# Kernel optimization log

Measured on AMD Instinct MI355X. Metric: run time of the kernel, lower is better.

Reference implementation:

```python
import jax, jax.numpy as jnp
import numpy as np

N, H, W, KB, CTRL, MEM, L, NMOD = 256, 14, 14, 512, 512, 512, 8, 9
TEMP = 1.0
EPS = 1e-12


def _l2norm(x):
    # torch F.normalize(p=2, dim=-1, eps=1e-12)
    return x / jnp.maximum(jnp.linalg.norm(x, axis=-1, keepdims=True), EPS)


def _spatial_softmax(att):  # [N,H,W,1]
    n = att.shape[0]
    return jax.nn.softmax(att.reshape(n, -1), axis=1).reshape(att.shape)


def _extract_softmax_avg(kb, att_raw):  # -> [N,KB]
    return (kb * _spatial_softmax(att_raw)).sum((1, 2))


def _move_bw(ptr):
    # conv1d with kernel [0,0,1], pad 1 => shift left (pop); guard keeps mass at slot 0
    new = jnp.pad(ptr[:, 1:], ((0, 0), (0, 1)))
    return new.at[:, 0].add(ptr[:, 0])


def _move_fw(ptr):
    # conv1d with kernel [1,0,0], pad 1 => shift right (push); guard keeps mass at slot L-1
    new = jnp.pad(ptr[:, :-1], ((0, 0), (1, 0)))
    return new.at[:, -1].add(ptr[:, -1])


def _read(stk, ptr):  # [N,H,W,L],[N,L] -> [N,H,W,1]
    return (stk * ptr[:, None, None, :]).sum(-1, keepdims=True)


def _write(stk, ptr, att):
    p = ptr[:, None, None, :]
    return att * p + stk * (1.0 - p)


def _sharpen(ptr):
    return jax.nn.softmax(ptr / TEMP, axis=1)


def setup_inputs() -> dict:
    key = jax.random.key(0)
    ks = jax.random.split(key, 16)

    def lin(k, fan_in, shape):
        return (jax.random.normal(k, shape, jnp.float32) / np.sqrt(fan_in)).astype(jnp.float32)

    u_ptr = jax.random.uniform(ks[0], (N, L), jnp.float32)
    u_mod = jax.random.uniform(ks[1], (N, NMOD), jnp.float32)
    C2 = 2 * KB + CTRL
    return {
        "control_state": jax.random.normal(ks[2], (N, CTRL), jnp.float32),
        "kb_batch": jax.random.normal(ks[3], (N, H, W, KB), jnp.float32),
        "module_prob": u_mod / u_mod.sum(1, keepdims=True),
        "mem_prev": jax.random.normal(ks[4], (N, MEM), jnp.float32),
        "att_stack_prev": jax.random.uniform(ks[5], (N, H, W, L), jnp.float32),
        "stack_ptr_prev": u_ptr / u_ptr.sum(1, keepdims=True),
        "find_ci_w": lin(ks[6], CTRL, (CTRL, KB)), "find_ci_b": jnp.zeros((KB,), jnp.float32),
        "find_conv_w": lin(ks[7], KB, (KB, 1)), "find_conv_b": jnp.zeros((1,), jnp.float32),
        "transform_ci_w": lin(ks[8], CTRL, (CTRL, KB)), "transform_ci_b": jnp.zeros((KB,), jnp.float32),
        "transform_conv_w": lin(ks[9], KB, (KB, 1)), "transform_conv_b": jnp.zeros((1,), jnp.float32),
        "scene_conv_w": lin(ks[10], KB, (KB, 1)), "scene_conv_b": jnp.zeros((1,), jnp.float32),
        "describeone_ci_w": lin(ks[11], CTRL, (CTRL, KB)), "describeone_ci_b": jnp.zeros((KB,), jnp.float32),
        "describeone_mem_w": lin(ks[12], C2, (C2, MEM)), "describeone_mem_b": jnp.zeros((MEM,), jnp.float32),
        "describetwo_ci_w": lin(ks[13], CTRL, (CTRL, KB)), "describetwo_ci_b": jnp.zeros((KB,), jnp.float32),
        "describetwo_mem_w": lin(ks[14], C2, (C2, MEM)), "describetwo_mem_b": jnp.zeros((MEM,), jnp.float32),
    }


def reference(control_state, kb_batch, module_prob, mem_prev, att_stack_prev, stack_ptr_prev,
              find_ci_w, find_ci_b, find_conv_w, find_conv_b,
              transform_ci_w, transform_ci_b, transform_conv_w, transform_conv_b,
              scene_conv_w, scene_conv_b,
              describeone_ci_w, describeone_ci_b, describeone_mem_w, describeone_mem_b,
              describetwo_ci_w, describetwo_ci_b, describetwo_mem_w, describetwo_mem_b):
    mem_zero = jnp.zeros_like(mem_prev)

    def NoOp(stk, ptr):
        return stk, ptr, mem_prev

    def Find(stk, ptr):
        c = control_state @ find_ci_w + find_ci_b  # [N,KB]
        elt = _l2norm(kb_batch * c[:, None, None, :])
        att = elt @ find_conv_w + find_conv_b  # 1x1 conv on channels-last -> [N,H,W,1]
        ptr = _move_fw(ptr)
        return _write(stk, ptr, att), ptr, mem_zero

    def Transform(stk, ptr):
        att_in = _read(stk, ptr)
        c = control_state @ transform_ci_w + transform_ci_b
        kb_att = _extract_softmax_avg(kb_batch, att_in)
        elt = _l2norm(kb_batch * c[:, None, None, :] * kb_att[:, None, None, :])
        att = elt @ transform_conv_w + transform_conv_b
        return _write(stk, ptr, att), ptr, mem_zero

    def And(stk, ptr):
        att2 = _read(stk, ptr)
        ptr = _move_bw(ptr)
        att1 = _read(stk, ptr)
        return _write(stk, ptr, jnp.minimum(att1, att2)), ptr, mem_zero

    def Or(stk, ptr):
        att2 = _read(stk, ptr)
        ptr = _move_bw(ptr)
        att1 = _read(stk, ptr)
        return _write(stk, ptr, jnp.maximum(att1, att2)), ptr, mem_zero

    def Filter(stk, ptr):
        stk, ptr, _ = Find(stk, ptr)
        stk, ptr, _ = And(stk, ptr)
        return stk, ptr, mem_zero

    def Scene(stk, ptr):
        att = _l2norm(kb_batch) @ scene_conv_w + scene_conv_b
        ptr = _move_fw(ptr)
        return _write(stk, ptr, att), ptr, mem_zero

    def DescribeOne(stk, ptr):
        att_in = _read(stk, ptr)
        c = control_state @ describeone_ci_w + describeone_ci_b
        kb_att = _extract_softmax_avg(kb_batch, att_in)
        elt = _l2norm(c * kb_att)
        mem = jnp.concatenate([control_state, elt, kb_att], axis=1) @ describeone_mem_w + describeone_mem_b
        return stk, ptr, mem

    def DescribeTwo(stk, ptr):
        att2 = _read(stk, ptr)
        ptr = _move_bw(ptr)
        att1 = _read(stk, ptr)
        c = control_state @ describetwo_ci_w + describetwo_ci_b
        kb_att1 = _extract_softmax_avg(kb_batch, att1)
        kb_att2 = _extract_softmax_avg(kb_batch, att2)
        elt = _l2norm(c * kb_att1 * kb_att2)
        mem = jnp.concatenate([control_state, elt, kb_att1], axis=1) @ describetwo_mem_w + describetwo_mem_b
        stk = _write(stk, ptr, jnp.minimum(att1, att2))
        return stk, ptr, mem

    funcs = [NoOp, Find, Transform, Filter, And, Or, Scene, DescribeOne, DescribeTwo]
    res = [f(att_stack_prev, stack_ptr_prev) for f in funcs]  # fixed small set of modules
    stks = jnp.stack([r[0] for r in res], axis=-1)  # [N,H,W,L,M]
    ptrs = jnp.stack([r[1] for r in res], axis=-1)  # [N,L,M]
    mems = jnp.stack([r[2] for r in res], axis=-1)  # [N,MEM,M]
    att_stack_avg = (module_prob[:, None, None, None, :] * stks).sum(-1)
    stack_ptr_avg = _sharpen((module_prob[:, None, :] * ptrs).sum(-1))
    mem_avg = (module_prob[:, None, :] * mems).sum(-1)
    return att_stack_avg, stack_ptr_avg, mem_avg
```

## Files before the change

kernel.cpp:

```cpp
#include <hip/hip_runtime.h>
#include <math.h>

constexpr int   NB   = 256;
constexpr int   HW   = 196;
constexpr int   KBC  = 512;
constexpr int   LSZ  = 8;
constexpr float EPSF = 1e-12f;

constexpr size_t S_ATT    = (size_t)NB * HW;
constexpr size_t OFF_ATT1 = 0;
constexpr size_t OFF_ATT2 = OFF_ATT1 + S_ATT;
constexpr size_t OFF_W1   = OFF_ATT2 + S_ATT;
constexpr size_t OFF_W2   = OFF_W1   + S_ATT;
constexpr size_t OFF_AF   = OFF_W2   + S_ATT;
constexpr size_t OFF_AT   = OFF_AF   + S_ATT;
constexpr size_t OFF_AS   = OFF_AT   + S_ATT;
constexpr size_t OFF_GP1  = OFF_AS   + S_ATT;
constexpr size_t OFF_KP   = OFF_GP1  + (size_t)4*NB*2048;
constexpr size_t OFF_A1   = OFF_KP   + (size_t)4*NB*1024;
constexpr size_t OFF_A2   = OFF_A1   + (size_t)NB*1536;
constexpr size_t OFF_G    = OFF_A2   + (size_t)NB*1536;
constexpr size_t OFF_P2   = OFF_G    + (size_t)NB*512;
constexpr size_t OFF_PF   = OFF_P2   + (size_t)16*NB*512;
constexpr size_t OFF_PB   = OFF_PF   + (size_t)NB*LSZ;
constexpr size_t OFF_PFB  = OFF_PB   + (size_t)NB*LSZ;
constexpr size_t OFF_SF2  = OFF_PFB  + (size_t)NB*LSZ;
constexpr size_t OFF_SFFB = OFF_SF2  + NB;
constexpr size_t WS_FLOATS= OFF_SFFB + NB;

static __device__ __forceinline__ float4 ld4(const float* p) {
    return *reinterpret_cast<const float4*>(p);
}

__global__ __launch_bounds__(256) void k_front(
    const float* __restrict__ stk, const float* __restrict__ ptrp,
    float* __restrict__ att1g, float* __restrict__ att2g,
    float* __restrict__ w1g, float* __restrict__ w2g,
    float* __restrict__ fws, float* __restrict__ bws, float* __restrict__ fbws,
    float* __restrict__ sf2ws, float* __restrict__ sffbws,
    const float* __restrict__ control,
    const float* __restrict__ B0, const float* __restrict__ B1,
    const float* __restrict__ B2, const float* __restrict__ B3,
    float* __restrict__ GP1)
{
    __shared__ float red[256];
    __shared__ float As[16][68];
    __shared__ float Bs[16][68];
    const int t = threadIdx.x;

    if (blockIdx.x < 256) {
        const int n = blockIdx.x;
        float pp[8], f[8], b[8], fb[8];
#pragma unroll
        for (int l = 0; l < 8; ++l) pp[l] = ptrp[n*8 + l];
        f[0] = 0.f;
#pragma unroll
        for (int l = 1; l < 8; ++l) f[l] = pp[l-1];
        f[7] += pp[7];
#pragma unroll
        for (int l = 0; l < 7; ++l) b[l] = pp[l+1];
        b[7] = 0.f;
        b[0] += pp[0];
#pragma unroll
        for (int l = 0; l < 7; ++l) fb[l] = f[l+1];
        fb[7] = 0.f;
        fb[0] += f[0];

        if (t == 0) {
            float sf2 = 0.f, sffb = 0.f;
#pragma unroll
            for (int l = 0; l < 8; ++l) {
                fws[n*8+l] = f[l]; bws[n*8+l] = b[l]; fbws[n*8+l] = fb[l];
                sf2  += f[l]*f[l];
                sffb += f[l]*fb[l];
            }
            sf2ws[n] = sf2; sffbws[n] = sffb;
        }

        float a1 = 0.f, a2 = 0.f;
        if (t < HW) {
            const float* sp = stk + ((size_t)n*HW + t) * 8;
            float4 v0 = ld4(sp), v1 = ld4(sp + 4);
            float s[8] = {v0.x, v0.y, v0.z, v0.w, v1.x, v1.y, v1.z, v1.w};
#pragma unroll
            for (int l = 0; l < 8; ++l) {
                a2 = fmaf(s[l], pp[l], a2);
                a1 = fmaf(s[l],  b[l], a1);
            }
            att1g[n*HW + t] = a1;
            att2g[n*HW + t] = a2;
        }

        red[t] = (t < HW) ? a1 : -3.0e38f;
        __syncthreads();
        for (int off = 128; off > 0; off >>= 1) { if (t < off) red[t] = fmaxf(red[t], red[t+off]); __syncthreads(); }
        const float m1 = red[0];
        __syncthreads();
        float e1 = (t < HW) ? __expf(a1 - m1) : 0.f;
        red[t] = e1;
        __syncthreads();
        for (int off = 128; off > 0; off >>= 1) { if (t < off) red[t] += red[t+off]; __syncthreads(); }
        const float s1 = red[0];
        __syncthreads();
        if (t < HW) w1g[n*HW + t] = e1 / s1;

        red[t] = (t < HW) ? a2 : -3.0e38f;
        __syncthreads();
        for (int off = 128; off > 0; off >>= 1) { if (t < off) red[t] = fmaxf(red[t], red[t+off]); __syncthreads(); }
        const float m2 = red[0];
        __syncthreads();
        float e2 = (t < HW) ? __expf(a2 - m2) : 0.f;
        red[t] = e2;
        __syncthreads();
        for (int off = 128; off > 0; off >>= 1) { if (t < off) red[t] += red[t+off]; __syncthreads(); }
        const float s2 = red[0];
        __syncthreads();
        if (t < HW) w2g[n*HW + t] = e2 / s2;
        return;
    }

    const int idx = blockIdx.x - 256;
    const int bn = (idx & 31) * 64;
    const int bm = ((idx >> 5) & 3) * 64;
    const int ks = idx >> 7;
    const int mat = bn >> 9;
    const float* B = (mat == 0) ? B0 : (mat == 1) ? B1 : (mat == 2) ? B2 : B3;
    const int kbase = ks * 128;
    const int bcol = bn & 511;

    const int tx = t & 15, ty = t >> 4;
    float acc[4][4] = {};
    const int ar = t >> 2, ac4 = (t & 3) * 4;
    const int br = t >> 4, bc4 = (t & 15) * 4;
    const float* Aptr = control + (size_t)(bm + ar) * 512 + kbase + ac4;
    const float* Bptr = B + (size_t)(kbase + br) * 512 + bcol + bc4;

    float4 aR = ld4(Aptr), bR = ld4(Bptr);
    for (int tile = 0; tile < 8; ++tile) {
        As[ac4+0][ar] = aR.x; As[ac4+1][ar] = aR.y; As[ac4+2][ar] = aR.z; As[ac4+3][ar] = aR.w;
        *reinterpret_cast<float4*>(&Bs[br][bc4]) = bR;
        __syncthreads();
        if (tile + 1 < 8) {
            aR = ld4(Aptr + (tile+1)*16);
            bR = ld4(Bptr + (size_t)(tile+1)*16*512);
        }
#pragma unroll
        for (int k = 0; k < 16; ++k) {
            float4 ra = *reinterpret_cast<const float4*>(&As[k][ty*4]);
            float4 rb = *reinterpret_cast<const float4*>(&Bs[k][tx*4]);
            const float av[4] = {ra.x, ra.y, ra.z, ra.w};
            const float bv[4] = {rb.x, rb.y, rb.z, rb.w};
#pragma unroll
            for (int i = 0; i < 4; ++i)
#pragma unroll
                for (int j = 0; j < 4; ++j)
                    acc[i][j] = fmaf(av[i], bv[j], acc[i][j]);
        }
        __syncthreads();
    }
#pragma unroll
    for (int i = 0; i < 4; ++i) {
        float4 v = make_float4(acc[i][0], acc[i][1], acc[i][2], acc[i][3]);
        *reinterpret_cast<float4*>(&GP1[((size_t)ks*NB + bm + ty*4 + i) * 2048 + bn + tx*4]) = v;
    }
}

__global__ __launch_bounds__(256) void k_kbA(
    const float* __restrict__ kb, const float* __restrict__ GP1,
    const float* __restrict__ find_ci_b,
    const float* __restrict__ w_find, const float* __restrict__ b_find,
    const float* __restrict__ w_scene, const float* __restrict__ b_scene,
    const float* __restrict__ w1g, const float* __restrict__ w2g,
    float* __restrict__ aF, float* __restrict__ aS, float* __restrict__ kpart)
{
    const int blk = blockIdx.x;
    const int n = blk >> 2, sp = blk & 3;
    const int t = threadIdx.x, wv = t >> 6, lane = t & 63;
    const int k0 = lane * 8;
    const int p0 = sp * 49;

    __shared__ float w1s[49], w2s[49];
    __shared__ float kred[4][1024];
    if (t < 49) { w1s[t] = w1g[n*HW + p0 + t]; w2s[t] = w2g[n*HW + p0 + t]; }
    __syncthreads();

    float cf[8], wf[8], wsc[8];
    {
        const float* gp = GP1 + (size_t)n*2048 + k0;
        float4 a0 = ld4(gp),            a1 = ld4(gp + 4);
        float4 b0 = ld4(gp + 524288),   b1 = ld4(gp + 524288 + 4);
        float4 c0 = ld4(gp + 1048576),  c1 = ld4(gp + 1048576 + 4);
        float4 d0 = ld4(gp + 1572864),  d1 = ld4(gp + 1572864 + 4);
        float4 e0 = ld4(find_ci_b + k0), e1 = ld4(find_ci_b + k0 + 4);
        cf[0]=a0.x+b0.x+c0.x+d0.x+e0.x; cf[1]=a0.y+b0.y+c0.y+d0.y+e0.y;
        cf[2]=a0.z+b0.z+c0.z+d0.z+e0.z; cf[3]=a0.w+b0.w+c0.w+d0.w+e0.w;
        cf[4]=a1.x+b1.x+c1.x+d1.x+e1.x; cf[5]=a1.y+b1.y+c1.y+d1.y+e1.y;
        cf[6]=a1.z+b1.z+c1.z+d1.z+e1.z; cf[7]=a1.w+b1.w+c1.w+d1.w+e1.w;
        float4 f0 = ld4(w_find + k0), f1 = ld4(w_find + k0 + 4);
        wf[0]=f0.x; wf[1]=f0.y; wf[2]=f0.z; wf[3]=f0.w; wf[4]=f1.x; wf[5]=f1.y; wf[6]=f1.z; wf[7]=f1.w;
        float4 g0 = ld4(w_scene + k0), g1 = ld4(w_scene + k0 + 4);
        wsc[0]=g0.x; wsc[1]=g0.y; wsc[2]=g0.z; wsc[3]=g0.w; wsc[4]=g1.x; wsc[5]=g1.y; wsc[6]=g1.z; wsc[7]=g1.w;
    }
    const float bf = b_find[0], bs = b_scene[0];

    float k1a[8] = {0,0,0,0,0,0,0,0};
    float k2a[8] = {0,0,0,0,0,0,0,0};

    const float* src0 = kb + (((size_t)n*HW + p0 + wv) * KBC + k0);
    float4 v0 = ld4(src0), v1 = ld4(src0 + 4);
    for (int pl = wv; pl < 49; pl += 4) {
        float4 n0, n1;
        if (pl + 4 < 49) {
            const float* ns = kb + (((size_t)n*HW + p0 + pl + 4) * KBC + k0);
            n0 = ld4(ns); n1 = ld4(ns + 4);
        }
        float kv[8] = {v0.x, v0.y, v0.z, v0.w, v1.x, v1.y, v1.z, v1.w};
        float sA = 0.f, sB = 0.f, sE = 0.f, sF = 0.f;
#pragma unroll
        for (int j = 0; j < 8; ++j) {
            const float t1 = kv[j] * cf[j];
            sA = fmaf(t1, t1, sA);
            sB = fmaf(t1, wf[j], sB);
            sE = fmaf(kv[j], kv[j], sE);
            sF = fmaf(kv[j], wsc[j], sF);
        }
        const float w1p = w1s[pl], w2p = w2s[pl];
#pragma unroll
        for (int j = 0; j < 8; ++j) {
            k1a[j] = fmaf(w1p, kv[j], k1a[j]);
            k2a[j] = fmaf(w2p, kv[j], k2a[j]);
        }
#pragma unroll
        for (int m = 1; m < 64; m <<= 1) {
            sA += __shfl_xor(sA, m);
            sB += __shfl_xor(sB, m);
            sE += __shfl_xor(sE, m);
            sF += __shfl_xor(sF, m);
        }
        if (lane == 0) {
            const size_t p = (size_t)n*HW + p0 + pl;
            aF[p] = sB / fmaxf(sqrtf(sA), EPSF) + bf;
            aS[p] = sF / fmaxf(sqrtf(sE), EPSF) + bs;
        }
        v0 = n0; v1 = n1;
    }
#pragma unroll
    for (int j = 0; j < 8; ++j) { kred[wv][k0 + j] = k1a[j]; kred[wv][512 + k0 + j] = k2a[j]; }
    __syncthreads();
    for (int idx = t; idx < 1024; idx += 256) {
        const float s = kred[0][idx] + kred[1][idx] + kred[2][idx] + kred[3][idx];
        kpart[((size_t)sp*NB + n) * 1024 + idx] = s;
    }
}

__global__ __launch_bounds__(256) void k_elt(
    const float* __restrict__ kpart, const float* __restrict__ GP1,
    const float* __restrict__ tr_ci_b, const float* __restrict__ d1_ci_b,
    const float* __restrict__ d2_ci_b,
    const float* __restrict__ control, const float* __restrict__ prob,
    float* __restrict__ g, float* __restrict__ A1, float* __restrict__ A2)
{
    const int n = blockIdx.x;
    const int t = threadIdx.x;
    __shared__ float k1s[512], k2s[512];
    for (int idx = t; idx < 512; idx += 256) {
        float s1 = 0.f, s2 = 0.f;
#pragma unroll
        for (int sp = 0; sp < 4; ++sp) {
            const float* base = kpart + ((size_t)sp*NB + n) * 1024;
            s1 += base[idx];
            s2 += base[512 + idx];
        }
        k1s[idx] = s1; k2s[idx] = s2;
    }
    __syncthreads();

    float v1[2], v2[2];
    float sum1 = 0.f, sum2 = 0.f;
#pragma unroll
    for (int i = 0; i < 2; ++i) {
        const int k = t + i*256;
        const float* gp = GP1 + (size_t)n*2048 + k;
        const float ct  = gp[512]  + gp[524288+512]  + gp[1048576+512]  + gp[1572864+512]  + tr_ci_b[k];
        const float cd1 = gp[1024] + gp[524288+1024] + gp[1048576+1024] + gp[1572864+1024] + d1_ci_b[k];
        const float cd2 = gp[1536] + gp[524288+1536] + gp[1048576+1536] + gp[1572864+1536] + d2_ci_b[k];
        g[(size_t)n*512 + k] = ct * k2s[k];
        v1[i] = cd1 * k2s[k];
        v2[i] = cd2 * k1s[k] * k2s[k];
        sum1 = fmaf(v1[i], v1[i], sum1);
        sum2 = fmaf(v2[i], v2[i], sum2);
    }
    __shared__ float r1[256], r2[256];
    r1[t] = sum1; r2[t] = sum2;
    __syncthreads();
    for (int off = 128; off > 0; off >>= 1) {
        if (t < off) { r1[t] += r1[t+off]; r2[t] += r2[t+off]; }
        __syncthreads();
    }
    const float n1 = fmaxf(sqrtf(r1[0]), EPSF);
    const float n2 = fmaxf(sqrtf(r2[0]), EPSF);
    const float p7 = prob[n*9 + 7], p8 = prob[n*9 + 8];
#pragma unroll
    for (int i = 0; i < 2; ++i) {
        const int k = t + i*256;
        const float c = control[(size_t)n*512 + k];
        A1[(size_t)n*1536 + k]        = p7 * c;
        A1[(size_t)n*1536 + 512 + k]  = p7 * v1[i] / n1;
        A1[(size_t)n*1536 + 1024 + k] = p7 * k2s[k];
        A2[(size_t)n*1536 + k]        = p8 * c;
        A2[(size_t)n*1536 + 512 + k]  = p8 * v2[i] / n2;
        A2[(size_t)n*1536 + 1024 + k] = p8 * k1s[k];
    }
}

__global__ __launch_bounds__(256) void k_mid(
    const float* __restrict__ kb, const float* __restrict__ g,
    const float* __restrict__ w_tr, const float* __restrict__ b_tr,
    float* __restrict__ aT,
    const float* __restrict__ A1, const float* __restrict__ A2,
    const float* __restrict__ W1, const float* __restrict__ W2,
    float* __restrict__ P2)
{
    __shared__ float As[16][68];
    __shared__ float Bs[16][68];
    const int t = threadIdx.x;
    const int g3 = blockIdx.x / 3, r3 = blockIdx.x % 3;

    if (r3 != 0) {
        const int kidx = g3 * 2 + (r3 - 1);
        const int n = kidx >> 2, sp = kidx & 3;
        const int wv = t >> 6, lane = t & 63;
        const int k0 = lane * 8;
        const int p0 = sp * 49;
        float gv[8], wt[8];
        {
            float4 a0 = ld4(g + (size_t)n*512 + k0), a1 = ld4(g + (size_t)n*512 + k0 + 4);
            gv[0]=a0.x; gv[1]=a0.y; gv[2]=a0.z; gv[3]=a0.w; gv[4]=a1.x; gv[5]=a1.y; gv[6]=a1.z; gv[7]=a1.w;
            float4 b0 = ld4(w_tr + k0), b1 = ld4(w_tr + k0 + 4);
            wt[0]=b0.x; wt[1]=b0.y; wt[2]=b0.z; wt[3]=b0.w; wt[4]=b1.x; wt[5]=b1.y; wt[6]=b1.z; wt[7]=b1.w;
        }
        const float bt = b_tr[0];
        const float* src0 = kb + (((size_t)n*HW + p0 + wv) * KBC + k0);
        float4 v0 = ld4(src0), v1 = ld4(src0 + 4);
        for (int pl = wv; pl < 49; pl += 4) {
            float4 n0, n1;
            if (pl + 4 < 49) {
                const float* ns = kb + (((size_t)n*HW + p0 + pl + 4) * KBC + k0);
                n0 = ld4(ns); n1 = ld4(ns + 4);
            }
            float kv[8] = {v0.x, v0.y, v0.z, v0.w, v1.x, v1.y, v1.z, v1.w};
            float sC = 0.f, sD = 0.f;
#pragma unroll
            for (int j = 0; j < 8; ++j) {
                const float u = kv[j] * gv[j];
                sC = fmaf(u, u, sC);
                sD = fmaf(u, wt[j], sD);
            }
#pragma unroll
            for (int m = 1; m < 64; m <<= 1) { sC += __shfl_xor(sC, m); sD += __shfl_xor(sD, m); }
            if (lane == 0) aT[(size_t)n*HW + p0 + pl] = sD / fmaxf(sqrtf(sC), EPSF) + bt;
            v0 = n0; v1 = n1;
        }
        return;
    }

    const int idx = g3;
    const int bn = (idx & 7) * 64;
    const int bm = ((idx >> 3) & 3) * 64;
    const int ks = idx >> 5;
    const int mat = ks >> 3;
    const float* A = mat ? A2 : A1;
    const float* B = mat ? W2 : W1;
    const int kbase = ks * 192 - mat * 1536;

    const int tx = t & 15, ty = t >> 4;
    float acc[4][4] = {};
    const int ar = t >> 2, ac4 = (t & 3) * 4;
    const int br = t >> 4, bc4 = (t & 15) * 4;
    const float* Aptr = A + (size_t)(bm + ar) * 1536 + kbase + ac4;
    const float* Bptr = B + (size_t)(kbase + br) * 512 + bn + bc4;

    float4 aR = ld4(Aptr), bR = ld4(Bptr);
    for (int tile = 0; tile < 12; ++tile) {
        As[ac4+0][ar] = aR.x; As[ac4+1][ar] = aR.y; As[ac4+2][ar] = aR.z; As[ac4+3][ar] = aR.w;
        *reinterpret_cast<float4*>(&Bs[br][bc4]) = bR;
        __syncthreads();
        if (tile + 1 < 12) {
            aR = ld4(Aptr + (tile+1)*16);
            bR = ld4(Bptr + (size_t)(tile+1)*16*512);
        }
#pragma unroll
        for (int k = 0; k < 16; ++k) {
            float4 ra = *reinterpret_cast<const float4*>(&As[k][ty*4]);
            float4 rb = *reinterpret_cast<const float4*>(&Bs[k][tx*4]);
            const float av[4] = {ra.x, ra.y, ra.z, ra.w};
            const float bv[4] = {rb.x, rb.y, rb.z, rb.w};
#pragma unroll
            for (int i = 0; i < 4; ++i)
#pragma unroll
                for (int j = 0; j < 4; ++j)
                    acc[i][j] = fmaf(av[i], bv[j], acc[i][j]);
        }
        __syncthreads();
    }
#pragma unroll
    for (int i = 0; i < 4; ++i) {
        float4 v = make_float4(acc[i][0], acc[i][1], acc[i][2], acc[i][3]);
        *reinterpret_cast<float4*>(&P2[((size_t)ks*NB + bm + ty*4 + i) * 512 + bn + tx*4]) = v;
    }
}

__global__ __launch_bounds__(256) void k_back(
    const float* __restrict__ P2, const float* __restrict__ memprev,
    const float* __restrict__ prob,
    const float* __restrict__ mb1, const float* __restrict__ mb2,
    float* __restrict__ out_mem,
    const float* __restrict__ stk, const float* __restrict__ ptrp,
    const float* __restrict__ att1g, const float* __restrict__ att2g,
    const float* __restrict__ aFg, const float* __restrict__ aTg, const float* __restrict__ aSg,
    const float* __restrict__ fws, const float* __restrict__ bws, const float* __restrict__ fbws,
    const float* __restrict__ sf2ws, const float* __restrict__ sffbws,
    float* __restrict__ out_att, float* __restrict__ out_ptr)
{
    const int t = threadIdx.x;
    if (blockIdx.x < 128) {
        const size_t q = ((size_t)blockIdx.x * 256 + t) * 4;
        const int n = (int)(q >> 9), j = (int)(q & 511);
        const float p0 = prob[n*9 + 0], p7 = prob[n*9 + 7], p8 = prob[n*9 + 8];
        float4 s = ld4(P2 + q);
#pragma unroll
        for (int sp = 1; sp < 16; ++sp) {
            float4 v = ld4(P2 + (size_t)sp*131072 + q);
            s.x += v.x; s.y += v.y; s.z += v.z; s.w += v.w;
        }
        float4 mp = ld4(memprev + q);
        float4 w1 = ld4(mb1 + j), w2 = ld4(mb2 + j);
        float4 o;
        o.x = p0*mp.x + s.x + p7*w1.x + p8*w2.x;
        o.y = p0*mp.y + s.y + p7*w1.y + p8*w2.y;
        o.z = p0*mp.z + s.z + p7*w1.z + p8*w2.z;
        o.w = p0*mp.w + s.w + p7*w1.w + p8*w2.w;
        *reinterpret_cast<float4*>(&out_mem[q]) = o;
        return;
    }

    const int n = blockIdx.x - 128;
    __shared__ float pp[8], f[8], b[8], fb[8], pr[9], sc2[2];
    if (t < 8) { pp[t] = ptrp[n*8+t]; f[t] = fws[n*8+t]; b[t] = bws[n*8+t]; fb[t] = fbws[n*8+t]; }
    if (t < 9) pr[t] = prob[n*9+t];
    if (t == 0) { sc2[0] = sf2ws[n]; sc2[1] = sffbws[n]; }
    __syncthreads();

    if (t < HW) {
        const size_t p = (size_t)n*HW + t;
        const float* spt = stk + p*8;
        float4 v0 = ld4(spt), v1 = ld4(spt+4);
        float s[8] = {v0.x, v0.y, v0.z, v0.w, v1.x, v1.y, v1.z, v1.w};
        const float a1 = att1g[p], a2 = att2g[p];
        const float vaF = aFg[p], vaT = aTg[p], vaS = aSg[p];
        const float mn = fminf(a1, a2), mx = fmaxf(a1, a2);
        float rf = 0.f, rf2 = 0.f, rfb = 0.f, rffb = 0.f;
#pragma unroll
        for (int l = 0; l < 8; ++l) {
            rf   = fmaf(s[l], f[l],        rf);
            rf2  = fmaf(s[l], f[l]*f[l],   rf2);
            rfb  = fmaf(s[l], fb[l],       rfb);
            rffb = fmaf(s[l], f[l]*fb[l],  rffb);
        }
        const float att2p = vaF*sc2[0] + rf  - rf2;
        const float att1p = vaF*sc2[1] + rfb - rffb;
        const float mnF = fminf(att1p, att2p);
        const float c48 = pr[4] + pr[8];
        float o[8];
#pragma unroll
        for (int l = 0; l < 8; ++l) {
            const float sl = s[l];
            const float stkF = vaF*f[l] + sl*(1.f - f[l]);
            float r = (pr[0] + pr[7]) * sl;
            r = fmaf(pr[1], stkF, r);
            r = fmaf(pr[2], vaT*pp[l] + sl*(1.f - pp[l]), r);
            r = fmaf(pr[3], mnF*fb[l] + stkF*(1.f - fb[l]), r);
            r = fmaf(c48,   mn*b[l] + sl*(1.f - b[l]), r);
            r = fmaf(pr[5], mx*b[l] + sl*(1.f - b[l]), r);
            r = fmaf(pr[6], vaS*f[l] + sl*(1.f - f[l]), r);
            o[l] = r;
        }
        *reinterpret_cast<float4*>(out_att + p*8)     = make_float4(o[0], o[1], o[2], o[3]);
        *reinterpret_cast<float4*>(out_att + p*8 + 4) = make_float4(o[4], o[5], o[6], o[7]);
    }

    if (t == 0) {
        const float cpp = pr[0] + pr[2] + pr[7];
        const float cf  = pr[1] + pr[6];
        const float cb  = pr[4] + pr[5] + pr[8];
        float pa[8];
        float m = -3.0e38f;
#pragma unroll
        for (int l = 0; l < 8; ++l) {
            pa[l] = cpp*pp[l] + cf*f[l] + cb*b[l] + pr[3]*fb[l];
            m = fmaxf(m, pa[l]);
        }
        float ssum = 0.f;
#pragma unroll
        for (int l = 0; l < 8; ++l) { pa[l] = __expf(pa[l] - m); ssum += pa[l]; }
#pragma unroll
        for (int l = 0; l < 8; ++l) out_ptr[n*8 + l] = pa[l] / ssum;
    }
}

extern "C" void kernel_launch(void* const* d_in, const int* in_sizes, int n_in,
                              void* d_out, int out_size, void* d_ws, size_t ws_size,
                              hipStream_t stream)
{
    (void)in_sizes; (void)n_in; (void)out_size;
    const float* control = (const float*)d_in[0];
    const float* kb      = (const float*)d_in[1];
    const float* prob    = (const float*)d_in[2];
    const float* memprev = (const float*)d_in[3];
    const float* stk     = (const float*)d_in[4];
    const float* ptrp    = (const float*)d_in[5];
    const float* find_w  = (const float*)d_in[6];
    const float* find_b  = (const float*)d_in[7];
    const float* findc_w = (const float*)d_in[8];
    const float* findc_b = (const float*)d_in[9];
    const float* tr_w    = (const float*)d_in[10];
    const float* tr_b    = (const float*)d_in[11];
    const float* trc_w   = (const float*)d_in[12];
    const float* trc_b   = (const float*)d_in[13];
    const float* sc_w    = (const float*)d_in[14];
    const float* sc_b    = (const float*)d_in[15];
    const float* d1_w    = (const float*)d_in[16];
    const float* d1_b    = (const float*)d_in[17];
    const float* d1m_w   = (const float*)d_in[18];
    const float* d1m_b   = (const float*)d_in[19];
    const float* d2_w    = (const float*)d_in[20];
    const float* d2_b    = (const float*)d_in[21];
    const float* d2m_w   = (const float*)d_in[22];
    const float* d2m_b   = (const float*)d_in[23];

    if (ws_size < WS_FLOATS * sizeof(float)) return;

    float* ws    = (float*)d_ws;
    float* att1g = ws + OFF_ATT1;
    float* att2g = ws + OFF_ATT2;
    float* w1g   = ws + OFF_W1;
    float* w2g   = ws + OFF_W2;
    float* aF    = ws + OFF_AF;
    float* aT    = ws + OFF_AT;
    float* aS    = ws + OFF_AS;
    float* GP1   = ws + OFF_GP1;
    float* kpart = ws + OFF_KP;
    float* A1    = ws + OFF_A1;
    float* A2    = ws + OFF_A2;
    float* g     = ws + OFF_G;
    float* P2    = ws + OFF_P2;
    float* fws   = ws + OFF_PF;
    float* bws   = ws + OFF_PB;
    float* fbws  = ws + OFF_PFB;
    float* sf2   = ws + OFF_SF2;
    float* sffb  = ws + OFF_SFFB;

    float* out_att = (float*)d_out;
    float* out_ptr = out_att + (size_t)NB*HW*LSZ;
    float* out_mem = out_ptr + (size_t)NB*LSZ;

    k_front<<<256 + 512, 256, 0, stream>>>(
        stk, ptrp, att1g, att2g, w1g, w2g, fws, bws, fbws, sf2, sffb,
        control, find_w, tr_w, d1_w, d2_w, GP1);
    k_kbA<<<NB*4, 256, 0, stream>>>(kb, GP1, find_b, findc_w, findc_b, sc_w, sc_b,
                                    w1g, w2g, aF, aS, kpart);
    k_elt<<<NB, 256, 0, stream>>>(kpart, GP1, tr_b, d1_b, d2_b,
                                  control, prob, g, A1, A2);
    k_mid<<<1536, 256, 0, stream>>>(kb, g, trc_w, trc_b, aT,
                                    A1, A2, d1m_w, d2m_w, P2);
    k_back<<<128 + 256, 256, 0, stream>>>(P2, memprev, prob, d1m_b, d2m_b, out_mem,
                                          stk, ptrp, att1g, att2g, aF, aT, aS,
                                          fws, bws, fbws, sf2, sffb, out_att, out_ptr);
}
```

Measured before the change: 78.49 us.

## Fuse back kernel into mid and front, atomic-accumulate mem GEMM output

Removes the k_back launch. The pointer-softmax moves into k_front, the mem base term into k_elt, and the att-stack blend into k_mid's kb blocks, which now keep aT in shared memory. The split-K for both GEMMs is halved (front 4→2 K-splits, mid 16→8), and the mid GEMM partials are added with atomics directly into out_mem instead of going through a P2 buffer. This saves one launch and the partial-sum round trips through global memory. In exchange, the GEMM blocks run longer with less parallelism, float atomics make the summation order nondeterministic, and k_front now interleaves softmax and GEMM blocks.

After: 95.87 us. +22.1%, slower.

```diff
diff --git a/kernel.cpp b/kernel.cpp
--- a/kernel.cpp
+++ b/kernel.cpp
@@ -13,15 +13,13 @@
 constexpr size_t OFF_W1   = OFF_ATT2 + S_ATT;
 constexpr size_t OFF_W2   = OFF_W1   + S_ATT;
 constexpr size_t OFF_AF   = OFF_W2   + S_ATT;
-constexpr size_t OFF_AT   = OFF_AF   + S_ATT;
-constexpr size_t OFF_AS   = OFF_AT   + S_ATT;
+constexpr size_t OFF_AS   = OFF_AF   + S_ATT;
 constexpr size_t OFF_GP1  = OFF_AS   + S_ATT;
-constexpr size_t OFF_KP   = OFF_GP1  + (size_t)4*NB*2048;
+constexpr size_t OFF_KP   = OFF_GP1  + (size_t)2*NB*2048;
 constexpr size_t OFF_A1   = OFF_KP   + (size_t)4*NB*1024;
 constexpr size_t OFF_A2   = OFF_A1   + (size_t)NB*1536;
 constexpr size_t OFF_G    = OFF_A2   + (size_t)NB*1536;
-constexpr size_t OFF_P2   = OFF_G    + (size_t)NB*512;
-constexpr size_t OFF_PF   = OFF_P2   + (size_t)16*NB*512;
+constexpr size_t OFF_PF   = OFF_G    + (size_t)NB*512;
 constexpr size_t OFF_PB   = OFF_PF   + (size_t)NB*LSZ;
 constexpr size_t OFF_PFB  = OFF_PB   + (size_t)NB*LSZ;
 constexpr size_t OFF_SF2  = OFF_PFB  + (size_t)NB*LSZ;
@@ -34,10 +32,12 @@
 
 __global__ __launch_bounds__(256) void k_front(
     const float* __restrict__ stk, const float* __restrict__ ptrp,
+    const float* __restrict__ prob,
     float* __restrict__ att1g, float* __restrict__ att2g,
     float* __restrict__ w1g, float* __restrict__ w2g,
     float* __restrict__ fws, float* __restrict__ bws, float* __restrict__ fbws,
     float* __restrict__ sf2ws, float* __restrict__ sffbws,
+    float* __restrict__ out_ptr,
     const float* __restrict__ control,
     const float* __restrict__ B0, const float* __restrict__ B1,
     const float* __restrict__ B2, const float* __restrict__ B3,
@@ -48,8 +48,8 @@
     __shared__ float Bs[16][68];
     const int t = threadIdx.x;
 
-    if (blockIdx.x < 256) {
-        const int n = blockIdx.x;
+    if ((blockIdx.x & 1) == 0) {
+        const int n = blockIdx.x >> 1;
         float pp[8], f[8], b[8], fb[8];
 #pragma unroll
         for (int l = 0; l < 8; ++l) pp[l] = ptrp[n*8 + l];
@@ -75,6 +75,24 @@
                 sffb += f[l]*fb[l];
             }
             sf2ws[n] = sf2; sffbws[n] = sffb;
+            float pr[9];
+#pragma unroll
+            for (int q = 0; q < 9; ++q) pr[q] = prob[n*9 + q];
+            const float cpp = pr[0] + pr[2] + pr[7];
+            const float cf  = pr[1] + pr[6];
+            const float cb  = pr[4] + pr[5] + pr[8];
+            float pa[8];
+            float m = -3.0e38f;
+#pragma unroll
+            for (int l = 0; l < 8; ++l) {
+                pa[l] = cpp*pp[l] + cf*f[l] + cb*b[l] + pr[3]*fb[l];
+                m = fmaxf(m, pa[l]);
+            }
+            float ssum = 0.f;
+#pragma unroll
+            for (int l = 0; l < 8; ++l) { pa[l] = __expf(pa[l] - m); ssum += pa[l]; }
+#pragma unroll
+            for (int l = 0; l < 8; ++l) out_ptr[n*8 + l] = pa[l] / ssum;
         }
 
         float a1 = 0.f, a2 = 0.f;
@@ -119,13 +137,13 @@
         return;
     }
 
-    const int idx = blockIdx.x - 256;
+    const int idx = blockIdx.x >> 1;
     const int bn = (idx & 31) * 64;
     const int bm = ((idx >> 5) & 3) * 64;
     const int ks = idx >> 7;
     const int mat = bn >> 9;
     const float* B = (mat == 0) ? B0 : (mat == 1) ? B1 : (mat == 2) ? B2 : B3;
-    const int kbase = ks * 128;
+    const int kbase = ks * 256;
     const int bcol = bn & 511;
 
     const int tx = t & 15, ty = t >> 4;
@@ -136,11 +154,11 @@
     const float* Bptr = B + (size_t)(kbase + br) * 512 + bcol + bc4;
 
     float4 aR = ld4(Aptr), bR = ld4(Bptr);
-    for (int tile = 0; tile < 8; ++tile) {
+    for (int tile = 0; tile < 16; ++tile) {
         As[ac4+0][ar] = aR.x; As[ac4+1][ar] = aR.y; As[ac4+2][ar] = aR.z; As[ac4+3][ar] = aR.w;
         *reinterpret_cast<float4*>(&Bs[br][bc4]) = bR;
         __syncthreads();
-        if (tile + 1 < 8) {
+        if (tile + 1 < 16) {
             aR = ld4(Aptr + (tile+1)*16);
             bR = ld4(Bptr + (size_t)(tile+1)*16*512);
         }
@@ -189,13 +207,11 @@
         const float* gp = GP1 + (size_t)n*2048 + k0;
         float4 a0 = ld4(gp),            a1 = ld4(gp + 4);
         float4 b0 = ld4(gp + 524288),   b1 = ld4(gp + 524288 + 4);
-        float4 c0 = ld4(gp + 1048576),  c1 = ld4(gp + 1048576 + 4);
-        float4 d0 = ld4(gp + 1572864),  d1 = ld4(gp + 1572864 + 4);
         float4 e0 = ld4(find_ci_b + k0), e1 = ld4(find_ci_b + k0 + 4);
-        cf[0]=a0.x+b0.x+c0.x+d0.x+e0.x; cf[1]=a0.y+b0.y+c0.y+d0.y+e0.y;
-        cf[2]=a0.z+b0.z+c0.z+d0.z+e0.z; cf[3]=a0.w+b0.w+c0.w+d0.w+e0.w;
-        cf[4]=a1.x+b1.x+c1.x+d1.x+e1.x; cf[5]=a1.y+b1.y+c1.y+d1.y+e1.y;
-        cf[6]=a1.z+b1.z+c1.z+d1.z+e1.z; cf[7]=a1.w+b1.w+c1.w+d1.w+e1.w;
+        cf[0]=a0.x+b0.x+e0.x; cf[1]=a0.y+b0.y+e0.y;
+        cf[2]=a0.z+b0.z+e0.z; cf[3]=a0.w+b0.w+e0.w;
+        cf[4]=a1.x+b1.x+e1.x; cf[5]=a1.y+b1.y+e1.y;
+        cf[6]=a1.z+b1.z+e1.z; cf[7]=a1.w+b1.w+e1.w;
         float4 f0 = ld4(w_find + k0), f1 = ld4(w_find + k0 + 4);
         wf[0]=f0.x; wf[1]=f0.y; wf[2]=f0.z; wf[3]=f0.w; wf[4]=f1.x; wf[5]=f1.y; wf[6]=f1.z; wf[7]=f1.w;
         float4 g0 = ld4(w_scene + k0), g1 = ld4(w_scene + k0 + 4);
@@ -258,7 +274,10 @@
     const float* __restrict__ tr_ci_b, const float* __restrict__ d1_ci_b,
     const float* __restrict__ d2_ci_b,
     const float* __restrict__ control, const float* __restrict__ prob,
-    float* __restrict__ g, float* __restrict__ A1, float* __restrict__ A2)
+    const float* __restrict__ memprev,
+    const float* __restrict__ mb1, const float* __restrict__ mb2,
+    float* __restrict__ g, float* __restrict__ A1, float* __restrict__ A2,
+    float* __restrict__ out_mem)
 {
     const int n = blockIdx.x;
     const int t = threadIdx.x;
@@ -275,20 +294,25 @@
     }
     __syncthreads();
 
+    const float p0m = prob[n*9 + 0];
+    const float p7 = prob[n*9 + 7], p8 = prob[n*9 + 8];
+
     float v1[2], v2[2];
     float sum1 = 0.f, sum2 = 0.f;
 #pragma unroll
     for (int i = 0; i < 2; ++i) {
         const int k = t + i*256;
         const float* gp = GP1 + (size_t)n*2048 + k;
-        const float ct  = gp[512]  + gp[524288+512]  + gp[1048576+512]  + gp[1572864+512]  + tr_ci_b[k];
-        const float cd1 = gp[1024] + gp[524288+1024] + gp[1048576+1024] + gp[1572864+1024] + d1_ci_b[k];
-        const float cd2 = gp[1536] + gp[524288+1536] + gp[1048576+1536] + gp[1572864+1536] + d2_ci_b[k];
+        const float ct  = gp[512]  + gp[524288+512]  + tr_ci_b[k];
+        const float cd1 = gp[1024] + gp[524288+1024] + d1_ci_b[k];
+        const float cd2 = gp[1536] + gp[524288+1536] + d2_ci_b[k];
         g[(size_t)n*512 + k] = ct * k2s[k];
         v1[i] = cd1 * k2s[k];
         v2[i] = cd2 * k1s[k] * k2s[k];
         sum1 = fmaf(v1[i], v1[i], sum1);
         sum2 = fmaf(v2[i], v2[i], sum2);
+        out_mem[(size_t)n*512 + k] = p0m * memprev[(size_t)n*512 + k]
+                                   + p7 * mb1[k] + p8 * mb2[k];
     }
     __shared__ float r1[256], r2[256];
     r1[t] = sum1; r2[t] = sum2;
@@ -299,7 +323,6 @@
     }
     const float n1 = fmaxf(sqrtf(r1[0]), EPSF);
     const float n2 = fmaxf(sqrtf(r2[0]), EPSF);
-    const float p7 = prob[n*9 + 7], p8 = prob[n*9 + 8];
 #pragma unroll
     for (int i = 0; i < 2; ++i) {
         const int k = t + i*256;
@@ -316,22 +339,36 @@
 __global__ __launch_bounds__(256) void k_mid(
     const float* __restrict__ kb, const float* __restrict__ g,
     const float* __restrict__ w_tr, const float* __restrict__ b_tr,
-    float* __restrict__ aT,
     const float* __restrict__ A1, const float* __restrict__ A2,
     const float* __restrict__ W1, const float* __restrict__ W2,
-    float* __restrict__ P2)
+    float* __restrict__ out_mem,
+    const float* __restrict__ stk, const float* __restrict__ ptrp,
+    const float* __restrict__ prob,
+    const float* __restrict__ att1g, const float* __restrict__ att2g,
+    const float* __restrict__ aFg, const float* __restrict__ aSg,
+    const float* __restrict__ fws, const float* __restrict__ bws,
+    const float* __restrict__ fbws,
+    const float* __restrict__ sf2ws, const float* __restrict__ sffbws,
+    float* __restrict__ out_att)
 {
     __shared__ float As[16][68];
     __shared__ float Bs[16][68];
+    __shared__ float aTs[49];
+    __shared__ float pps[8], fs[8], bs_[8], fbs[8], prs[9], sc2[2];
     const int t = threadIdx.x;
-    const int g3 = blockIdx.x / 3, r3 = blockIdx.x % 3;
-
-    if (r3 != 0) {
-        const int kidx = g3 * 2 + (r3 - 1);
+    const int g5 = blockIdx.x / 5, r5 = blockIdx.x % 5;
+
+    if (r5 != 0) {
+        const int kidx = g5 * 4 + (r5 - 1);
         const int n = kidx >> 2, sp = kidx & 3;
         const int wv = t >> 6, lane = t & 63;
         const int k0 = lane * 8;
         const int p0 = sp * 49;
+
+        if (t < 8) { pps[t] = ptrp[n*8+t]; fs[t] = fws[n*8+t]; bs_[t] = bws[n*8+t]; fbs[t] = fbws[n*8+t]; }
+        if (t < 9) prs[t] = prob[n*9+t];
+        if (t == 0) { sc2[0] = sf2ws[n]; sc2[1] = sffbws[n]; }
+
         float gv[8], wt[8];
         {
             float4 a0 = ld4(g + (size_t)n*512 + k0), a1 = ld4(g + (size_t)n*512 + k0 + 4);
@@ -358,20 +395,59 @@
             }
 #pragma unroll
             for (int m = 1; m < 64; m <<= 1) { sC += __shfl_xor(sC, m); sD += __shfl_xor(sD, m); }
-            if (lane == 0) aT[(size_t)n*HW + p0 + pl] = sD / fmaxf(sqrtf(sC), EPSF) + bt;
+            if (lane == 0) aTs[pl] = sD / fmaxf(sqrtf(sC), EPSF) + bt;
             v0 = n0; v1 = n1;
         }
+        __syncthreads();
+
+        if (t < 49) {
+            const size_t p = (size_t)n*HW + p0 + t;
+            const float* spt = stk + p*8;
+            float4 s0 = ld4(spt), s1v = ld4(spt+4);
+            float s[8] = {s0.x, s0.y, s0.z, s0.w, s1v.x, s1v.y, s1v.z, s1v.w};
+            const float a1 = att1g[p], a2 = att2g[p];
+            const float vaF = aFg[p], vaT = aTs[t], vaS = aSg[p];
+            const float mn = fminf(a1, a2), mx = fmaxf(a1, a2);
+            float rf = 0.f, rf2 = 0.f, rfb = 0.f, rffb = 0.f;
+#pragma unroll
+            for (int l = 0; l < 8; ++l) {
+                rf   = fmaf(s[l], fs[l],         rf);
+                rf2  = fmaf(s[l], fs[l]*fs[l],   rf2);
+                rfb  = fmaf(s[l], fbs[l],        rfb);
+                rffb = fmaf(s[l], fs[l]*fbs[l],  rffb);
+            }
+            const float att2p = vaF*sc2[0] + rf  - rf2;
+            const float att1p = vaF*sc2[1] + rfb - rffb;
+            const float mnF = fminf(att1p, att2p);
+            const float c48 = prs[4] + prs[8];
+            float o[8];
+#pragma unroll
+            for (int l = 0; l < 8; ++l) {
+                const float sl = s[l];
+                const float stkF = vaF*fs[l] + sl*(1.f - fs[l]);
+                float r = (prs[0] + prs[7]) * sl;
+                r = fmaf(prs[1], stkF, r);
+                r = fmaf(prs[2], vaT*pps[l] + sl*(1.f - pps[l]), r);
+                r = fmaf(prs[3], mnF*fbs[l] + stkF*(1.f - fbs[l]), r);
+                r = fmaf(c48,    mn*bs_[l] + sl*(1.f - bs_[l]), r);
+                r = fmaf(prs[5], mx*bs_[l] + sl*(1.f - bs_[l]), r);
+                r = fmaf(prs[6], vaS*fs[l] + sl*(1.f - fs[l]), r);
+                o[l] = r;
+            }
+            *reinterpret_cast<float4*>(out_att + p*8)     = make_float4(o[0], o[1], o[2], o[3]);
+            *reinterpret_cast<float4*>(out_att + p*8 + 4) = make_float4(o[4], o[5], o[6], o[7]);
+        }
         return;
     }
 
-    const int idx = g3;
+    const int idx = g5;
     const int bn = (idx & 7) * 64;
     const int bm = ((idx >> 3) & 3) * 64;
     const int ks = idx >> 5;
-    const int mat = ks >> 3;
+    const int mat = ks >> 2;
     const float* A = mat ? A2 : A1;
     const float* B = mat ? W2 : W1;
-    const int kbase = ks * 192 - mat * 1536;
+    const int kbase = ks * 384 - mat * 1536;
 
     const int tx = t & 15, ty = t >> 4;
     float acc[4][4] = {};
@@ -381,11 +457,11 @@
     const float* Bptr = B + (size_t)(kbase + br) * 512 + bn + bc4;
 
     float4 aR = ld4(Aptr), bR = ld4(Bptr);
-    for (int tile = 0; tile < 12; ++tile) {
+    for (int tile = 0; tile < 24; ++tile) {
         As[ac4+0][ar] = aR.x; As[ac4+1][ar] = aR.y; As[ac4+2][ar] = aR.z; As[ac4+3][ar] = aR.w;
         *reinterpret_cast<float4*>(&Bs[br][bc4]) = bR;
         __syncthreads();
-        if (tile + 1 < 12) {
+        if (tile + 1 < 24) {
             aR = ld4(Aptr + (tile+1)*16);
             bR = ld4(Bptr + (size_t)(tile+1)*16*512);
         }
@@ -405,106 +481,10 @@
     }
 #pragma unroll
     for (int i = 0; i < 4; ++i) {
-        float4 v = make_float4(acc[i][0], acc[i][1], acc[i][2], acc[i][3]);
-        *reinterpret_cast<float4*>(&P2[((size_t)ks*NB + bm + ty*4 + i) * 512 + bn + tx*4]) = v;
-    }
-}
-
-__global__ __launch_bounds__(256) void k_back(
-    const float* __restrict__ P2, const float* __restrict__ memprev,
-    const float* __restrict__ prob,
-    const float* __restrict__ mb1, const float* __restrict__ mb2,
-    float* __restrict__ out_mem,
-    const float* __restrict__ stk, const float* __restrict__ ptrp,
-    const float* __restrict__ att1g, const float* __restrict__ att2g,
-    const float* __restrict__ aFg, const float* __restrict__ aTg, const float* __restrict__ aSg,
-    const float* __restrict__ fws, const float* __restrict__ bws, const float* __restrict__ fbws,
-    const float* __restrict__ sf2ws, const float* __restrict__ sffbws,
-    float* __restrict__ out_att, float* __restrict__ out_ptr)
-{
-    const int t = threadIdx.x;
-    if (blockIdx.x < 128) {
-        const size_t q = ((size_t)blockIdx.x * 256 + t) * 4;
-        const int n = (int)(q >> 9), j = (int)(q & 511);
-        const float p0 = prob[n*9 + 0], p7 = prob[n*9 + 7], p8 = prob[n*9 + 8];
-        float4 s = ld4(P2 + q);
-#pragma unroll
-        for (int sp = 1; sp < 16; ++sp) {
-            float4 v = ld4(P2 + (size_t)sp*131072 + q);
-            s.x += v.x; s.y += v.y; s.z += v.z; s.w += v.w;
-        }
-        float4 mp = ld4(memprev + q);
-        float4 w1 = ld4(mb1 + j), w2 = ld4(mb2 + j);
-        float4 o;
-        o.x = p0*mp.x + s.x + p7*w1.x + p8*w2.x;
-        o.y = p0*mp.y + s.y + p7*w1.y + p8*w2.y;
-        o.z = p0*mp.z + s.z + p7*w1.z + p8*w2.z;
-        o.w = p0*mp.w + s.w + p7*w1.w + p8*w2.w;
-        *reinterpret_cast<float4*>(&out_mem[q]) = o;
-        return;
-    }
-
-    const int n = blockIdx.x - 128;
-    __shared__ float pp[8], f[8], b[8], fb[8], pr[9], sc2[2];
-    if (t < 8) { pp[t] = ptrp[n*8+t]; f[t] = fws[n*8+t]; b[t] = bws[n*8+t]; fb[t] = fbws[n*8+t]; }
-    if (t < 9) pr[t] = prob[n*9+t];
-    if (t == 0) { sc2[0] = sf2ws[n]; sc2[1] = sffbws[n]; }
-    __syncthreads();
-
-    if (t < HW) {
-        const size_t p = (size_t)n*HW + t;
-        const float* spt = stk + p*8;
-        float4 v0 = ld4(spt), v1 = ld4(spt+4);
-        float s[8] = {v0.x, v0.y, v0.z, v0.w, v1.x, v1.y, v1.z, v1.w};
-        const float a1 = att1g[p], a2 = att2g[p];
-        const float vaF = aFg[p], vaT = aTg[p], vaS = aSg[p];
-        const float mn = fminf(a1, a2), mx = fmaxf(a1, a2);
-        float rf = 0.f, rf2 = 0.f, rfb = 0.f, rffb = 0.f;
-#pragma unroll
-        for (int l = 0; l < 8; ++l) {
-            rf   = fmaf(s[l], f[l],        rf);
-            rf2  = fmaf(s[l], f[l]*f[l],   rf2);
-            rfb  = fmaf(s[l], fb[l],       rfb);
-            rffb = fmaf(s[l], f[l]*fb[l],  rffb);
-        }
-        const float att2p = vaF*sc2[0] + rf  - rf2;
-        const float att1p = vaF*sc2[1] + rfb - rffb;
-        const float mnF = fminf(att1p, att2p);
-        const float c48 = pr[4] + pr[8];
-        float o[8];
-#pragma unroll
-        for (int l = 0; l < 8; ++l) {
-            const float sl = s[l];
-            const float stkF = vaF*f[l] + sl*(1.f - f[l]);
-            float r = (pr[0] + pr[7]) * sl;
-            r = fmaf(pr[1], stkF, r);
-            r = fmaf(pr[2], vaT*pp[l] + sl*(1.f - pp[l]), r);
-            r = fmaf(pr[3], mnF*fb[l] + stkF*(1.f - fb[l]), r);
-            r = fmaf(c48,   mn*b[l] + sl*(1.f - b[l]), r);
-            r = fmaf(pr[5], mx*b[l] + sl*(1.f - b[l]), r);
-            r = fmaf(pr[6], vaS*f[l] + sl*(1.f - f[l]), r);
-            o[l] = r;
-        }
-        *reinterpret_cast<float4*>(out_att + p*8)     = make_float4(o[0], o[1], o[2], o[3]);
-        *reinterpret_cast<float4*>(out_att + p*8 + 4) = make_float4(o[4], o[5], o[6], o[7]);
-    }
-
-    if (t == 0) {
-        const float cpp = pr[0] + pr[2] + pr[7];
-        const float cf  = pr[1] + pr[6];
-        const float cb  = pr[4] + pr[5] + pr[8];
-        float pa[8];
-        float m = -3.0e38f;
-#pragma unroll
-        for (int l = 0; l < 8; ++l) {
-            pa[l] = cpp*pp[l] + cf*f[l] + cb*b[l] + pr[3]*fb[l];
-            m = fmaxf(m, pa[l]);
-        }
-        float ssum = 0.f;
-#pragma unroll
-        for (int l = 0; l < 8; ++l) { pa[l] = __expf(pa[l] - m); ssum += pa[l]; }
-#pragma unroll
-        for (int l = 0; l < 8; ++l) out_ptr[n*8 + l] = pa[l] / ssum;
+        float* dst = out_mem + (size_t)(bm + ty*4 + i) * 512 + bn + tx*4;
+#pragma unroll
+        for (int j = 0; j < 4; ++j)
+            unsafeAtomicAdd(dst + j, acc[i][j]);
     }
 }
 
@@ -546,14 +526,12 @@
     float* w1g   = ws + OFF_W1;
     float* w2g   = ws + OFF_W2;
     float* aF    = ws + OFF_AF;
-    float* aT    = ws + OFF_AT;
     float* aS    = ws + OFF_AS;
     float* GP1   = ws + OFF_GP1;
     float* kpart = ws + OFF_KP;
     float* A1    = ws + OFF_A1;
     float* A2    = ws + OFF_A2;
     float* g     = ws + OFF_G;
-    float* P2    = ws + OFF_P2;
     float* fws   = ws + OFF_PF;
     float* bws   = ws + OFF_PB;
     float* fbws  = ws + OFF_PFB;
@@ -564,16 +542,16 @@
     float* out_ptr = out_att + (size_t)NB*HW*LSZ;
     float* out_mem = out_ptr + (size_t)NB*LSZ;
 
-    k_front<<<256 + 512, 256, 0, stream>>>(
-        stk, ptrp, att1g, att2g, w1g, w2g, fws, bws, fbws, sf2, sffb,
-        control, find_w, tr_w, d1_w, d2_w, GP1);
+    k_front<<<512, 256, 0, stream>>>(
+        stk, ptrp, prob, att1g, att2g, w1g, w2g, fws, bws, fbws, sf2, sffb,
+        out_ptr, control, find_w, tr_w, d1_w, d2_w, GP1);
     k_kbA<<<NB*4, 256, 0, stream>>>(kb, GP1, find_b, findc_w, findc_b, sc_w, sc_b,
                                     w1g, w2g, aF, aS, kpart);
     k_elt<<<NB, 256, 0, stream>>>(kpart, GP1, tr_b, d1_b, d2_b,
-                                  control, prob, g, A1, A2);
-    k_mid<<<1536, 256, 0, stream>>>(kb, g, trc_w, trc_b, aT,
-                                    A1, A2, d1m_w, d2m_w, P2);
-    k_back<<<128 + 256, 256, 0, stream>>>(P2, memprev, prob, d1m_b, d2m_b, out_mem,
-                                          stk, ptrp, att1g, att2g, aF, aT, aS,
-                                          fws, bws, fbws, sf2, sffb, out_att, out_ptr);
+                                  control, prob, memprev, d1m_b, d2m_b,
+                                  g, A1, A2, out_mem);
+    k_mid<<<1280, 256, 0, stream>>>(kb, g, trc_w, trc_b,
+                                    A1, A2, d1m_w, d2m_w, out_mem,
+                                    stk, ptrp, prob, att1g, att2g, aF, aS,
+                                    fws, bws, fbws, sf2, sffb, out_att);
 }
```
